# Kernel optimization log

Hardware: AMD Instinct MI355X
Metric: run time of the kernel (lower is better)

The kernel has to match this reference:

```python
import jax, jax.numpy as jnp
import numpy as np

D_MODEL = 1024
N_HEADS = 16
D_K = D_MODEL // N_HEADS
THETA = 10000.0
SEQ = 2048
BATCH = 2


def setup_inputs() -> dict:
    key = jax.random.key(0)
    ks = jax.random.split(key, 5)
    std = (2.0 / (D_MODEL + D_MODEL)) ** 0.5
    return {
        "x": jax.random.normal(ks[0], (BATCH, SEQ, D_MODEL), dtype=jnp.float32),
        "token_positions": jnp.arange(SEQ, dtype=jnp.int64 if jax.config.jax_enable_x64 else jnp.int32),
        "wq": jax.random.normal(ks[1], (D_MODEL, D_MODEL), dtype=jnp.float32) * std,
        "wk": jax.random.normal(ks[2], (D_MODEL, D_MODEL), dtype=jnp.float32) * std,
        "wv": jax.random.normal(ks[3], (D_MODEL, D_MODEL), dtype=jnp.float32) * std,
        "wo": jax.random.normal(ks[4], (D_MODEL, D_MODEL), dtype=jnp.float32) * std,
    }


def _apply_rope(t, token_positions):
    # t: [b, h, s, d_k]; interleaved even/odd rotation (RoPE)
    k = jnp.arange(D_K // 2, dtype=t.dtype)
    inv_freq = THETA ** (-2.0 * k / D_K)                     # [d_k/2]
    angles = token_positions.astype(t.dtype)[:, None] * inv_freq  # [s, d_k/2]
    cos, sin = jnp.cos(angles), jnp.sin(angles)
    even, odd = t[..., 0::2], t[..., 1::2]
    re = even * cos - odd * sin
    ro = odd * cos + even * sin
    # re-interleave: stack last then reshape back to [..., d_k]
    return jnp.stack([re, ro], axis=-1).reshape(t.shape)


def reference(x, token_positions, wq, wk, wv, wo):
    b, s, _ = x.shape
    def proj(w):
        y = jnp.einsum("bsd,ed->bse", x, w)               # Linear: x @ W^T
        return y.reshape(b, s, N_HEADS, D_K).transpose(0, 2, 1, 3)  # [b,h,s,dk]
    q, k, v = proj(wq), proj(wk), proj(wv)
    q = _apply_rope(q, token_positions)
    k = _apply_rope(k, token_positions)
    scores = jnp.einsum("bhqd,bhkd->bhqk", q, k) / jnp.sqrt(jnp.asarray(D_K, x.dtype))
    attn = jax.nn.softmax(scores, axis=-1)
    out = jnp.einsum("bhqk,bhkd->bhqd", attn, v)          # [b,h,s,dk]
    out = out.transpose(0, 2, 1, 3).reshape(b, s, D_MODEL)
    return jnp.einsum("bsd,ed->bse", out, wo)
```

## Files before the change

kernel.cpp:

```cpp
#include <hip/hip_runtime.h>
#include <stdint.h>

typedef __bf16 bf16x8 __attribute__((ext_vector_type(8)));
typedef __bf16 bf16x2 __attribute__((ext_vector_type(2)));
typedef float f32x4 __attribute__((ext_vector_type(4)));
typedef float f32x16 __attribute__((ext_vector_type(16)));
typedef unsigned short ushort_t;
typedef unsigned int uint;
typedef uint uint4v __attribute__((ext_vector_type(4)));

#define SEQ    2048
#define DMODEL 1024
#define NHEAD  16
#define DKH    64
#define NBATCH 2
#define MROWS  (NBATCH*SEQ)
#define LOG2E  1.44269504088896340736f

__device__ __forceinline__ uint pk2(float a, float b) {
  bf16x2 t; t[0] = (__bf16)a; t[1] = (__bf16)b;
  return __builtin_bit_cast(uint, t);
}
__device__ __forceinline__ ushort_t b1(float a) {
  return __builtin_bit_cast(ushort_t, (__bf16)a);
}
__device__ __forceinline__ float fexp2(float x) {
#if __has_builtin(__builtin_amdgcn_exp2f)
  return __builtin_amdgcn_exp2f(x);
#else
  return exp2f(x);
#endif
}

__device__ __forceinline__ void gload16(const void* g, void* l) {
  __builtin_amdgcn_global_load_lds(
      (const __attribute__((address_space(1))) void*)g,
      (__attribute__((address_space(3))) void*)l, 16, 0, 0);
}

__device__ __forceinline__ f32x4 mfma16(bf16x8 a, bf16x8 b, f32x4 c) {
  return __builtin_amdgcn_mfma_f32_16x16x32_bf16(a, b, c, 0, 0, 0);
}
__device__ __forceinline__ f32x16 mfma32(bf16x8 a, bf16x8 b, f32x16 c) {
  return __builtin_amdgcn_mfma_f32_32x32x16_bf16(a, b, c, 0, 0, 0);
}

__global__ __launch_bounds__(256) void cvt_all(
    const float* __restrict__ x, const float* __restrict__ wq,
    const float* __restrict__ wk, const float* __restrict__ wv,
    const float* __restrict__ wo, uint2* __restrict__ out)
{
  int b = blockIdx.x;
  const float4* src; uint2* dst; int i;
  if (b < 4096) {
    i = b * 256 + threadIdx.x; src = (const float4*)x; dst = out;
  } else {
    int s = (b - 4096) >> 10;
    i = ((b - 4096) & 1023) * 256 + threadIdx.x;
    src = (const float4*)(s == 0 ? wq : s == 1 ? wk : s == 2 ? wv : wo);
    dst = out + (size_t)1048576 + (size_t)s * 262144;
  }
  float4 v = src[i];
  uint2 r; r.x = pk2(v.x, v.y); r.y = pk2(v.z, v.w);
  dst[i] = r;
}

__global__ __launch_bounds__(256) void rope_tab_kernel(const int* __restrict__ tokpos, float2* __restrict__ tab) {
  int t = blockIdx.x * 256 + threadIdx.x;
  int s = t >> 5, k = t & 31;
  double inv = pow(10000.0, -(double)(2 * k) / 64.0);
  double ang = (double)tokpos[s] * inv;
  tab[t] = make_float2((float)cos(ang), (float)sin(ang));
}

__global__ __launch_bounds__(256) void gemm_nt(
    const ushort_t* __restrict__ A, const ushort_t* __restrict__ W,
    const float2* __restrict__ tab,
    ushort_t* __restrict__ Qo, ushort_t* __restrict__ Ko, ushort_t* __restrict__ Vo,
    float* __restrict__ outf, int fused)
{
  __shared__ ushort_t lA[2][128 * 64];
  __shared__ ushort_t lB[2][128 * 64];
  const int tid = threadIdx.x;
  const int w = tid >> 6, l = tid & 63, lo = l & 15, hi = l >> 4;
  const int wr = (w >> 1) * 64, wc = (w & 1) * 64;
  const char* Ab = (const char*)A + (size_t)blockIdx.y * 128 * 2048;
  const char* Bb = (const char*)W + (size_t)blockIdx.x * 128 * 2048;
  f32x4 acc[4][4] = {};

  const int o0 = w * 1024 + l * 16;
  const int r0 = o0 >> 7;
  const int us = ((o0 >> 4) & 7) ^ (r0 & 7);
  const char* ap = Ab + (size_t)r0 * 2048 + us * 16;
  const char* bp = Bb + (size_t)r0 * 2048 + us * 16;

  auto stage = [&](char* dA, char* dB, const char* aq, const char* bq) {
    #pragma unroll
    for (int i = 0; i < 4; ++i) {
      gload16(aq + i * 65536, dA + w * 1024 + i * 4096);
      gload16(bq + i * 65536, dB + w * 1024 + i * 4096);
    }
  };
  auto comp = [&](const ushort_t* lAb, const ushort_t* lBb) {
    #pragma unroll
    for (int c = 0; c < 2; ++c) {
      bf16x8 af[4], wf[4];
      #pragma unroll
      for (int m = 0; m < 4; ++m) {
        int row = wr + m * 16 + lo;
        af[m] = *(const bf16x8*)((const char*)lAb + row * 128 + ((c * 64 + hi * 16) ^ ((row & 7) << 4)));
      }
      #pragma unroll
      for (int n = 0; n < 4; ++n) {
        int row = wc + n * 16 + lo;
        wf[n] = *(const bf16x8*)((const char*)lBb + row * 128 + ((c * 64 + hi * 16) ^ ((row & 7) << 4)));
      }
      #pragma unroll
      for (int m = 0; m < 4; ++m)
        #pragma unroll
        for (int n = 0; n < 4; ++n)
          acc[m][n] = mfma16(af[m], wf[n], acc[m][n]);
    }
  };

  stage((char*)lA[0], (char*)lB[0], ap, bp); ap += 128; bp += 128;
  __syncthreads();
  for (int it = 0; it < 16; it += 2) {
    stage((char*)lA[1], (char*)lB[1], ap, bp); ap += 128; bp += 128;
    comp(lA[0], lB[0]);
    __syncthreads();
    if (it + 2 < 16) { stage((char*)lA[0], (char*)lB[0], ap, bp); ap += 128; bp += 128; }
    comp(lA[1], lB[1]);
    __syncthreads();
  }

  const int mode = fused ? (blockIdx.x >> 3) : 3;
  const int colblk = fused ? (blockIdx.x & 7) : blockIdx.x;
  const int rowbase = blockIdx.y * 128 + wr + hi * 4;
  const int colbase = colblk * 128 + wc + lo;

  if (mode == 3) {
    #pragma unroll
    for (int m = 0; m < 4; ++m)
      #pragma unroll
      for (int n = 0; n < 4; ++n) {
        int e = colbase + n * 16;
        #pragma unroll
        for (int r = 0; r < 4; ++r) {
          int row = rowbase + m * 16 + r;
          outf[(size_t)row * 1024 + e] = acc[m][n][r];
        }
      }
    return;
  }
  if (mode == 2) {
    #pragma unroll
    for (int m = 0; m < 4; ++m) {
      int row0 = rowbase + m * 16;
      int b = row0 >> 11, s = row0 & 2047;
      int b2 = (s >> 2) & 3;
      int sp = (s & ~12) | ((b2 & 1) << 3) | ((b2 >> 1) << 2);
      #pragma unroll
      for (int n = 0; n < 4; ++n) {
        int e = colbase + n * 16;
        int h = e >> 6, dk = e & 63;
        uint2 pk;
        pk.x = pk2(acc[m][n][0], acc[m][n][1]);
        pk.y = pk2(acc[m][n][2], acc[m][n][3]);
        *(uint2*)(Vo + ((size_t)((b * NHEAD + h) * DKH + dk) * SEQ + sp)) = pk;
      }
    }
    return;
  }
  ushort_t* outb = (mode == 0) ? Qo : Ko;
  const float qscale = (mode == 0) ? (0.125f * LOG2E) : 1.0f;
  #pragma unroll
  for (int m = 0; m < 4; ++m) {
    #pragma unroll
    for (int n = 0; n < 4; ++n) {
      int e = colbase + n * 16;
      int h = e >> 6, dk = e & 63, kf = dk >> 1;
      float sgn = (e & 1) ? 1.0f : -1.0f;
      #pragma unroll
      for (int r = 0; r < 4; ++r) {
        int row = rowbase + m * 16 + r;
        int s = row & 2047, b = row >> 11;
        float2 cs = tab[s * 32 + kf];
        float v = acc[m][n][r];
        float p = __shfl_xor(v, 1, 64);
        float res = (v * cs.x + sgn * p * cs.y) * qscale;
        outb[((size_t)((b * NHEAD + h) * SEQ + s)) * DKH + dk] = b1(res);
      }
    }
  }
}

__global__ __launch_bounds__(256) void attn_fwd(
    const ushort_t* __restrict__ Qg, const ushort_t* __restrict__ Kg,
    const ushort_t* __restrict__ VTg, ushort_t* __restrict__ attn)
{
  __shared__ char lds[49152];
  const int tid = threadIdx.x;
  const int w = tid >> 6, l = tid & 63;
  const int qh = w >> 1, kp = w & 1;
  const int q31 = l & 31, hf = l >> 5, s7 = l & 7;
  const int bh = blockIdx.y;
  const int q0 = blockIdx.x * 128 + qh * 64;
  const char* Kb = (const char*)Kg + (size_t)bh * 2048 * 128;
  const char* Vb = (const char*)VTg + (size_t)bh * 64 * 4096;

  bf16x8 qreg[2][4];
  #pragma unroll
  for (int qb = 0; qb < 2; ++qb) {
    const ushort_t* qp = Qg + ((size_t)bh * 2048 + q0 + qb * 32 + q31) * 64 + hf * 8;
    #pragma unroll
    for (int c = 0; c < 4; ++c) qreg[qb][c] = *(const bf16x8*)(qp + c * 16);
  }

  f32x16 accO[2][2] = {};
  float lsum[2] = {0.f, 0.f};

  const char* ra[4];
  #pragma unroll
  for (int c = 0; c < 4; ++c)
    ra[c] = lds + q31 * 128 + ((c * 32 + hf * 16) ^ (s7 << 4));
  const int bq = kp * 8192;

  const int srow = tid >> 3, sw = (tid & 7) * 16;
  const int wl = sw ^ ((srow & 7) << 4);
  const char* ksp = Kb + (size_t)srow * 128 + wl;
  const char* vsp = Vb + (size_t)(srow + ((wl >> 6) & 1) * 32) * 4096 + (wl & 63);

  auto stageT = [&](int slot) {
    gload16(ksp,        lds + slot + tid * 16);
    gload16(ksp + 4096, lds + slot + 8192 + tid * 16);
    gload16(vsp,        lds + slot + 4096 + tid * 16);
    gload16(vsp + 64,   lds + slot + 12288 + tid * 16);
    ksp += 8192; vsp += 128;
  };

  auto tileC = [&](int slot) {
    const int bo = slot + bq;
    bf16x8 kf[4];
    #pragma unroll
    for (int c = 0; c < 4; ++c)
      kf[c] = *(const bf16x8*)(ra[c] + bo);
    f32x16 s0 = {}, s1 = {};
    #pragma unroll
    for (int c = 0; c < 4; ++c) {
      s0 = mfma32(kf[c], qreg[0][c], s0);
      s1 = mfma32(kf[c], qreg[1][c], s1);
    }
    float p0[16], p1[16];
    float t0 = 0.f, t1 = 0.f;
    #pragma unroll
    for (int r = 0; r < 16; ++r) { p0[r] = fexp2(s0[r]); t0 += p0[r]; }
    #pragma unroll
    for (int r = 0; r < 16; ++r) { p1[r] = fexp2(s1[r]); t1 += p1[r]; }
    lsum[0] += t0; lsum[1] += t1;
    #pragma unroll
    for (int kcl = 0; kcl < 2; ++kcl) {
      const float* a0 = p0 + kcl * 8;
      const float* a1 = p1 + kcl * 8;
      uint4v u0 = { pk2(a0[0], a0[1]), pk2(a0[2], a0[3]),
                    pk2(a0[4], a0[5]), pk2(a0[6], a0[7]) };
      uint4v u1 = { pk2(a1[0], a1[1]), pk2(a1[2], a1[3]),
                    pk2(a1[4], a1[5]), pk2(a1[6], a1[7]) };
      bf16x8 pb0 = __builtin_bit_cast(bf16x8, u0);
      bf16x8 pb1 = __builtin_bit_cast(bf16x8, u1);
      bf16x8 vf0 = *(const bf16x8*)(ra[kcl]     + bo + 4096);
      bf16x8 vf1 = *(const bf16x8*)(ra[kcl + 2] + bo + 4096);
      accO[0][0] = mfma32(vf0, pb0, accO[0][0]);
      accO[0][1] = mfma32(vf1, pb0, accO[0][1]);
      accO[1][0] = mfma32(vf0, pb1, accO[1][0]);
      accO[1][1] = mfma32(vf1, pb1, accO[1][1]);
    }
  };

  stageT(0);
  stageT(16384);
  #pragma unroll 1
  for (int it = 0; it < 10; ++it) {
    #pragma unroll
    for (int j = 0; j < 3; ++j) {
      asm volatile("s_waitcnt vmcnt(4)" ::: "memory");
      __builtin_amdgcn_s_barrier();
      __builtin_amdgcn_sched_barrier(0);
      stageT(((j + 2) % 3) * 16384);
      tileC(j * 16384);
    }
  }
  asm volatile("s_waitcnt vmcnt(4)" ::: "memory");
  __builtin_amdgcn_s_barrier();
  __builtin_amdgcn_sched_barrier(0);
  tileC(0);
  asm volatile("s_waitcnt vmcnt(0)" ::: "memory");
  __builtin_amdgcn_s_barrier();
  __builtin_amdgcn_sched_barrier(0);
  tileC(16384);

  __syncthreads();
  if (kp) {
    char* dst = lds + qh * 16384;
    #pragma unroll
    for (int qb = 0; qb < 2; ++qb)
      #pragma unroll
      for (int db = 0; db < 2; ++db)
        #pragma unroll
        for (int c2 = 0; c2 < 4; ++c2) {
          int j = qb * 8 + db * 4 + c2;
          f32x4 v = { accO[qb][db][c2 * 4 + 0], accO[qb][db][c2 * 4 + 1],
                      accO[qb][db][c2 * 4 + 2], accO[qb][db][c2 * 4 + 3] };
          *(f32x4*)(dst + j * 1024 + l * 16) = v;
        }
    *(float2*)(lds + 32768 + qh * 512 + l * 8) = make_float2(lsum[0], lsum[1]);
  }
  __syncthreads();
  if (!kp) {
    const char* srcp = lds + qh * 16384;
    #pragma unroll
    for (int qb = 0; qb < 2; ++qb)
      #pragma unroll
      for (int db = 0; db < 2; ++db)
        #pragma unroll
        for (int c2 = 0; c2 < 4; ++c2) {
          int j = qb * 8 + db * 4 + c2;
          f32x4 v = *(const f32x4*)(srcp + j * 1024 + l * 16);
          accO[qb][db][c2 * 4 + 0] += v[0];
          accO[qb][db][c2 * 4 + 1] += v[1];
          accO[qb][db][c2 * 4 + 2] += v[2];
          accO[qb][db][c2 * 4 + 3] += v[3];
        }
    float2 lo = *(const float2*)(lds + 32768 + qh * 512 + l * 8);
    lsum[0] += lo.x; lsum[1] += lo.y;

    int b = bh >> 4, head = bh & 15;
    #pragma unroll
    for (int qb = 0; qb < 2; ++qb) {
      float lt = lsum[qb] + __shfl_xor(lsum[qb], 32, 64);
      float inv = 1.0f / lt;
      ushort_t* op = attn + (size_t)(b * 2048 + q0 + qb * 32 + q31) * 1024 + head * 64;
      #pragma unroll
      for (int db = 0; db < 2; ++db)
        #pragma unroll
        for (int m = 0; m < 4; ++m) {
          int d0 = db * 32 + m * 8 + hf * 4;
          uint2 pk;
          pk.x = pk2(accO[qb][db][m * 4 + 0] * inv, accO[qb][db][m * 4 + 1] * inv);
          pk.y = pk2(accO[qb][db][m * 4 + 2] * inv, accO[qb][db][m * 4 + 3] * inv);
          *(uint2*)(op + d0) = pk;
        }
    }
  }
}

extern "C" void kernel_launch(void* const* d_in, const int* in_sizes, int n_in,
                              void* d_out, int out_size, void* d_ws, size_t ws_size,
                              hipStream_t stream) {
  const float* x  = (const float*)d_in[0];
  const int* tok  = (const int*)d_in[1];
  const float* wq = (const float*)d_in[2];
  const float* wk = (const float*)d_in[3];
  const float* wv = (const float*)d_in[4];
  const float* wo = (const float*)d_in[5];
  float* out = (float*)d_out;
  char* ws = (char*)d_ws;

  size_t off = 0;
  float2* tab = (float2*)(ws + off); off += (size_t)SEQ * 32 * sizeof(float2);
  ushort_t* xb  = (ushort_t*)(ws + off); off += (size_t)MROWS * DMODEL * 2;
  ushort_t* wqkv = (ushort_t*)(ws + off); off += (size_t)3 * DMODEL * DMODEL * 2;
  ushort_t* wob = (ushort_t*)(ws + off); off += (size_t)DMODEL * DMODEL * 2;
  ushort_t* Qg  = (ushort_t*)(ws + off); off += (size_t)MROWS * DMODEL * 2;
  ushort_t* Kg  = (ushort_t*)(ws + off); off += (size_t)MROWS * DMODEL * 2;
  ushort_t* VTg = (ushort_t*)(ws + off); off += (size_t)MROWS * DMODEL * 2;
  ushort_t* attnb = xb;
  if (ws_size < off) return;

  cvt_all<<<8192, 256, 0, stream>>>(x, wq, wk, wv, wo, (uint2*)xb);
  rope_tab_kernel<<<256, 256, 0, stream>>>(tok, tab);

  gemm_nt<<<dim3(24, 32), 256, 0, stream>>>(xb, wqkv, tab, Qg, Kg, VTg, nullptr, 1);

  attn_fwd<<<dim3(SEQ / 128, NBATCH * NHEAD), 256, 0, stream>>>(Qg, Kg, VTg, attnb);

  gemm_nt<<<dim3(8, 32), 256, 0, stream>>>(attnb, wob, nullptr, nullptr, nullptr, nullptr, out, 0);
}
```

Baseline: 129.7 us.

## Split attention keys across four independent waves with private LDS double buffers

```diff
diff --git a/kernel.cpp b/kernel.cpp
--- a/kernel.cpp
+++ b/kernel.cpp
@@ -199,13 +199,12 @@
     const ushort_t* __restrict__ Qg, const ushort_t* __restrict__ Kg,
     const ushort_t* __restrict__ VTg, ushort_t* __restrict__ attn)
 {
-  __shared__ char lds[49152];
+  __shared__ char lds[67584];
   const int tid = threadIdx.x;
   const int w = tid >> 6, l = tid & 63;
-  const int qh = w >> 1, kp = w & 1;
   const int q31 = l & 31, hf = l >> 5, s7 = l & 7;
   const int bh = blockIdx.y;
-  const int q0 = blockIdx.x * 128 + qh * 64;
+  const int q0 = blockIdx.x * 64;
   const char* Kb = (const char*)Kg + (size_t)bh * 2048 * 128;
   const char* Vb = (const char*)VTg + (size_t)bh * 64 * 4096;
 
@@ -220,27 +219,31 @@
   f32x16 accO[2][2] = {};
   float lsum[2] = {0.f, 0.f};
 
+  char* wlds = lds + w * 16384;
   const char* ra[4];
   #pragma unroll
   for (int c = 0; c < 4; ++c)
-    ra[c] = lds + q31 * 128 + ((c * 32 + hf * 16) ^ (s7 << 4));
-  const int bq = kp * 8192;
-
-  const int srow = tid >> 3, sw = (tid & 7) * 16;
-  const int wl = sw ^ ((srow & 7) << 4);
-  const char* ksp = Kb + (size_t)srow * 128 + wl;
-  const char* vsp = Vb + (size_t)(srow + ((wl >> 6) & 1) * 32) * 4096 + (wl & 63);
+    ra[c] = wlds + q31 * 128 + ((c * 32 + hf * 16) ^ (s7 << 4));
+
+  const int usw = (l & 7) ^ (l >> 3);
+  const int kb0 = w * 512;
+  const char* kst = Kb + (size_t)(kb0 + (l >> 3)) * 128 + usw * 16;
+  const char* vst = Vb + (size_t)((l >> 3) + (usw >> 2) * 32) * 4096
+                       + (size_t)kb0 * 2 + (usw & 3) * 16;
 
   auto stageT = [&](int slot) {
-    gload16(ksp,        lds + slot + tid * 16);
-    gload16(ksp + 4096, lds + slot + 8192 + tid * 16);
-    gload16(vsp,        lds + slot + 4096 + tid * 16);
-    gload16(vsp + 64,   lds + slot + 12288 + tid * 16);
-    ksp += 8192; vsp += 128;
+    char* sp = wlds + slot;
+    #pragma unroll
+    for (int i = 0; i < 4; ++i)
+      gload16(kst + i * 1024, sp + i * 1024 + l * 16);
+    #pragma unroll
+    for (int i = 0; i < 4; ++i)
+      gload16(vst + i * 32768, sp + 4096 + i * 1024 + l * 16);
+    kst += 4096; vst += 64;
   };
 
   auto tileC = [&](int slot) {
-    const int bo = slot + bq;
+    const int bo = slot;
     bf16x8 kf[4];
     #pragma unroll
     for (int c = 0; c < 4; ++c)
@@ -278,79 +281,70 @@
   };
 
   stageT(0);
-  stageT(16384);
   #pragma unroll 1
-  for (int it = 0; it < 10; ++it) {
-    #pragma unroll
-    for (int j = 0; j < 3; ++j) {
-      asm volatile("s_waitcnt vmcnt(4)" ::: "memory");
-      __builtin_amdgcn_s_barrier();
-      __builtin_amdgcn_sched_barrier(0);
-      stageT(((j + 2) % 3) * 16384);
-      tileC(j * 16384);
-    }
-  }
-  asm volatile("s_waitcnt vmcnt(4)" ::: "memory");
-  __builtin_amdgcn_s_barrier();
+  for (int it = 0; it < 7; ++it) {
+    asm volatile("s_waitcnt lgkmcnt(0)" ::: "memory");
+    stageT(8192);
+    asm volatile("s_waitcnt vmcnt(8)" ::: "memory");
+    __builtin_amdgcn_sched_barrier(0);
+    tileC(0);
+    asm volatile("s_waitcnt lgkmcnt(0)" ::: "memory");
+    stageT(0);
+    asm volatile("s_waitcnt vmcnt(8)" ::: "memory");
+    __builtin_amdgcn_sched_barrier(0);
+    tileC(8192);
+  }
+  asm volatile("s_waitcnt lgkmcnt(0)" ::: "memory");
+  stageT(8192);
+  asm volatile("s_waitcnt vmcnt(8)" ::: "memory");
   __builtin_amdgcn_sched_barrier(0);
   tileC(0);
   asm volatile("s_waitcnt vmcnt(0)" ::: "memory");
-  __builtin_amdgcn_s_barrier();
   __builtin_amdgcn_sched_barrier(0);
-  tileC(16384);
+  tileC(8192);
 
   __syncthreads();
-  if (kp) {
-    char* dst = lds + qh * 16384;
-    #pragma unroll
-    for (int qb = 0; qb < 2; ++qb)
-      #pragma unroll
-      for (int db = 0; db < 2; ++db)
-        #pragma unroll
-        for (int c2 = 0; c2 < 4; ++c2) {
-          int j = qb * 8 + db * 4 + c2;
-          f32x4 v = { accO[qb][db][c2 * 4 + 0], accO[qb][db][c2 * 4 + 1],
-                      accO[qb][db][c2 * 4 + 2], accO[qb][db][c2 * 4 + 3] };
-          *(f32x4*)(dst + j * 1024 + l * 16) = v;
-        }
-    *(float2*)(lds + 32768 + qh * 512 + l * 8) = make_float2(lsum[0], lsum[1]);
-  }
+  #pragma unroll
+  for (int qb = 0; qb < 2; ++qb)
+    #pragma unroll
+    for (int db = 0; db < 2; ++db)
+      #pragma unroll
+      for (int c2 = 0; c2 < 4; ++c2) {
+        int j = qb * 8 + db * 4 + c2;
+        f32x4 v = { accO[qb][db][c2 * 4 + 0], accO[qb][db][c2 * 4 + 1],
+                    accO[qb][db][c2 * 4 + 2], accO[qb][db][c2 * 4 + 3] };
+        *(f32x4*)(lds + w * 16384 + j * 1024 + l * 16) = v;
+      }
+  *(float2*)(lds + 65536 + w * 512 + l * 8) = make_float2(lsum[0], lsum[1]);
   __syncthreads();
-  if (!kp) {
-    const char* srcp = lds + qh * 16384;
-    #pragma unroll
-    for (int qb = 0; qb < 2; ++qb)
-      #pragma unroll
-      for (int db = 0; db < 2; ++db)
-        #pragma unroll
-        for (int c2 = 0; c2 < 4; ++c2) {
-          int j = qb * 8 + db * 4 + c2;
-          f32x4 v = *(const f32x4*)(srcp + j * 1024 + l * 16);
-          accO[qb][db][c2 * 4 + 0] += v[0];
-          accO[qb][db][c2 * 4 + 1] += v[1];
-          accO[qb][db][c2 * 4 + 2] += v[2];
-          accO[qb][db][c2 * 4 + 3] += v[3];
-        }
-    float2 lo = *(const float2*)(lds + 32768 + qh * 512 + l * 8);
-    lsum[0] += lo.x; lsum[1] += lo.y;
-
-    int b = bh >> 4, head = bh & 15;
-    #pragma unroll
-    for (int qb = 0; qb < 2; ++qb) {
-      float lt = lsum[qb] + __shfl_xor(lsum[qb], 32, 64);
-      float inv = 1.0f / lt;
-      ushort_t* op = attn + (size_t)(b * 2048 + q0 + qb * 32 + q31) * 1024 + head * 64;
-      #pragma unroll
-      for (int db = 0; db < 2; ++db)
-        #pragma unroll
-        for (int m = 0; m < 4; ++m) {
-          int d0 = db * 32 + m * 8 + hf * 4;
-          uint2 pk;
-          pk.x = pk2(accO[qb][db][m * 4 + 0] * inv, accO[qb][db][m * 4 + 1] * inv);
-          pk.y = pk2(accO[qb][db][m * 4 + 2] * inv, accO[qb][db][m * 4 + 3] * inv);
-          *(uint2*)(op + d0) = pk;
-        }
-    }
+
+  float lt0 = 0.f, lt1 = 0.f;
+  #pragma unroll
+  for (int wp = 0; wp < 4; ++wp) {
+    float2 lo = *(const float2*)(lds + 65536 + wp * 512 + l * 8);
+    lt0 += lo.x; lt1 += lo.y;
+  }
+  lt0 += __shfl_xor(lt0, 32, 64);
+  lt1 += __shfl_xor(lt1, 32, 64);
+  float inv0 = 1.0f / lt0, inv1 = 1.0f / lt1;
+  int b = bh >> 4, head = bh & 15;
+  #pragma unroll
+  for (int jj = 0; jj < 4; ++jj) {
+    int j = w * 4 + jj;
+    int qb = j >> 3, db = (j >> 2) & 1, c2 = j & 3;
+    f32x4 v = {0.f, 0.f, 0.f, 0.f};
+    #pragma unroll
+    for (int wp = 0; wp < 4; ++wp) {
+      f32x4 u = *(const f32x4*)(lds + wp * 16384 + j * 1024 + l * 16);
+      v[0] += u[0]; v[1] += u[1]; v[2] += u[2]; v[3] += u[3];
+    }
+    float inv = qb ? inv1 : inv0;
+    int d0 = db * 32 + c2 * 8 + hf * 4;
+    ushort_t* op = attn + (size_t)(b * 2048 + q0 + qb * 32 + q31) * 1024 + head * 64;
+    uint2 pk;
+    pk.x = pk2(v[0] * inv, v[1] * inv);
+    pk.y = pk2(v[2] * inv, v[3] * inv);
+    *(uint2*)(op + d0) = pk;
   }
 }
 
@@ -382,7 +376,7 @@
 
   gemm_nt<<<dim3(24, 32), 256, 0, stream>>>(xb, wqkv, tab, Qg, Kg, VTg, nullptr, 1);
 
-  attn_fwd<<<dim3(SEQ / 128, NBATCH * NHEAD), 256, 0, stream>>>(Qg, Kg, VTg, attnb);
+  attn_fwd<<<dim3(SEQ / 64, NBATCH * NHEAD), 256, 0, stream>>>(Qg, Kg, VTg, attnb);
 
   gemm_nt<<<dim3(8, 32), 256, 0, stream>>>(attnb, wob, nullptr, nullptr, nullptr, nullptr, out, 0);
 }
```

Result: no change. 130.3 us (+0.5%).
